# Kernel optimization log

Hardware: AMD Instinct MI355X
Metric: run time of the kernel (lower is better)

The kernel has to match this reference:

```python
import jax, jax.numpy as jnp
import numpy as np

IN_SLICE = (4, 4)   # input bit-plane widths, MSB first
W_SLICE = (4, 4)    # weight bit-plane widths, MSB first
KSIZE, STRIDE, PAD = 3, 1, 1
B, CIN, COUT, H, W = 16, 64, 128, 32, 32


def _slice_planes(x, bits):
    """Dynamic fixed-point quantization to sum(bits) signed bits, then split
    the magnitude into bit-planes (sign folded into each plane). Exact:
    sum_i 2**shift_i * plane_i == q, and scale * q ~= x."""
    n = int(sum(bits))
    qmax = float(2 ** (n - 1) - 1)
    scale = jnp.max(jnp.abs(x)) / qmax
    q = jnp.clip(jnp.round(x / scale), -qmax, qmax)
    sgn = jnp.sign(q)
    u = jnp.abs(q)
    planes, shifts = [], []
    s = n
    for b in bits:
        s -= b
        planes.append(sgn * (jnp.floor(u / (2.0 ** s)) % (2.0 ** b)))
        shifts.append(s)
    return planes, shifts, scale


def _unfold(x, k, stride, pad):
    """torch.nn.functional.unfold, (C, kh, kw) channel-major ordering.
    Returns [B, L, C*k*k], Ho, Wo."""
    b, c, h, w = x.shape
    xp = jnp.pad(x, ((0, 0), (0, 0), (pad, pad), (pad, pad)))
    ho = (h + 2 * pad - k) // stride + 1
    wo = (w + 2 * pad - k) // stride + 1
    cols = []
    for kh in range(k):
        for kw in range(k):
            cols.append(xp[:, :, kh:kh + (ho - 1) * stride + 1:stride,
                            kw:kw + (wo - 1) * stride + 1:stride])
    patches = jnp.stack(cols, axis=2)              # [B, C, k*k, Ho, Wo]
    patches = patches.reshape(b, c * k * k, ho * wo)
    return patches.transpose(0, 2, 1), ho, wo      # [B, L, K]


def _mem_conv(input, weight, bias):
    cout = weight.shape[0]
    wm = weight.reshape(cout, -1).T                # [K, Cout], matches weight.reshape(Cout,-1).t()
    xun, ho, wo = _unfold(input, KSIZE, STRIDE, PAD)
    xplanes, xshifts, xscale = _slice_planes(xun, IN_SLICE)
    wplanes, wshifts, wscale = _slice_planes(wm, W_SLICE)
    acc = jnp.zeros((input.shape[0], xun.shape[1], cout), dtype=input.dtype)
    for xp, sx in zip(xplanes, xshifts):
        for wp, sw in zip(wplanes, wshifts):
            # low-precision bit-plane GEMM with power-of-two shift recombination
            acc = acc + (2.0 ** (sx + sw)) * jnp.einsum('blk,ko->blo', xp, wp)
    out = (xscale * wscale) * acc                  # [B, L, Cout]
    out = out.transpose(0, 2, 1).reshape(input.shape[0], cout, ho, wo)
    return out + bias[None, :, None, None]


def setup_inputs() -> dict:
    key = jax.random.key(0)
    k1, k2, k3 = jax.random.split(key, 3)
    x = jax.random.normal(k1, (B, CIN, H, W), dtype=jnp.float32)
    fan_in = CIN * KSIZE * KSIZE
    bound = 1.0 / np.sqrt(fan_in)  # kaiming_uniform(a=sqrt(5)) -> U(-1/sqrt(fan_in), +)
    weight = jax.random.uniform(k2, (COUT, CIN, KSIZE, KSIZE), dtype=jnp.float32,
                                minval=-bound, maxval=bound)
    bias = jax.random.uniform(k3, (COUT,), dtype=jnp.float32, minval=-bound, maxval=bound)
    return {"input": x, "weight": weight, "bias": bias}


def reference(input, weight, bias):
    return _mem_conv(input, weight, bias)
```

## Files before the change

### kernel.cpp

```cpp
#include <hip/hip_runtime.h>

#define B_    16
#define CIN   64
#define COUT  128
#define H_    32
#define W_    32
#define HP    34
#define XCH   136
#define NPB   256

typedef __attribute__((ext_vector_type(4)))  int int4v;
typedef __attribute__((ext_vector_type(16))) int int16v;

__device__ __forceinline__ float wave_max256(const float* __restrict__ p) {
  const int lane = threadIdx.x & 63;
  float m = fmaxf(fmaxf(p[lane], p[lane + 64]),
                  fmaxf(p[lane + 128], p[lane + 192]));
#pragma unroll
  for (int off = 32; off > 0; off >>= 1)
    m = fmaxf(m, __shfl_down(m, off, 64));
  return __shfl(m, 0, 64);
}

__global__ __launch_bounds__(256) void maxabs_kernel(
    const float4* __restrict__ x4, const float4* __restrict__ w4,
    float* __restrict__ bmx, float* __restrict__ bmw) {
  const int nw4 = COUT * CIN * 9 / 4;
  const int tid = blockIdx.x * 256 + threadIdx.x;
  float mx = 0.0f, mw = 0.0f;
#pragma unroll
  for (int k = 0; k < 4; ++k) {
    float4 v = x4[tid + k * 65536];
    mx = fmaxf(mx, fmaxf(fmaxf(fabsf(v.x), fabsf(v.y)),
                         fmaxf(fabsf(v.z), fabsf(v.w))));
  }
  if (tid < nw4) {
    float4 v = w4[tid];
    mw = fmaxf(mw, fmaxf(fmaxf(fabsf(v.x), fabsf(v.y)),
                         fmaxf(fabsf(v.z), fabsf(v.w))));
  }
#pragma unroll
  for (int off = 32; off > 0; off >>= 1) {
    mx = fmaxf(mx, __shfl_down(mx, off, 64));
    mw = fmaxf(mw, __shfl_down(mw, off, 64));
  }
  __shared__ float smx[4], smw[4];
  const int wid = threadIdx.x >> 6;
  if ((threadIdx.x & 63) == 0) { smx[wid] = mx; smw[wid] = mw; }
  __syncthreads();
  if (threadIdx.x == 0) {
#pragma unroll
    for (int i = 1; i < 4; ++i) { mx = fmaxf(mx, smx[i]); mw = fmaxf(mw, smw[i]); }
    bmx[blockIdx.x] = mx;
    bmw[blockIdx.x] = mw;
  }
}

__global__ __launch_bounds__(256) void quant_pack_kernel(
    const float* __restrict__ x, const float* __restrict__ w,
    const float* __restrict__ bmx, const float* __restrict__ bmw,
    char* __restrict__ qx, char* __restrict__ qw) {
  __shared__ __align__(16) char lds[W_ * 80];
  const int t = threadIdx.x;
  const int bb = blockIdx.x;
  if (bb < 512) {
    const int b = bb >> 5, y = bb & 31;
    const float s = wave_max256(bmx) / 127.0f;
#pragma unroll
    for (int k = 0; k < 8; ++k) {
      const int u = t + k * 256;
      const int cin = u >> 5, xx = u & 31;
      float q = rintf(x[((b * CIN + cin) * H_ + y) * W_ + xx] / s);
      q = fminf(fmaxf(q, -127.0f), 127.0f);
      lds[xx * 80 + cin] = (char)(int)q;
    }
    __syncthreads();
    char* row = qx + (size_t)(b * HP + y + 1) * (XCH * 16);
    if (t < XCH) {
      const int c32 = t / 68;
      const int r   = t - c32 * 68;
      const int kb  = r / 34;
      const int xs  = r - kb * 34;
      uint4 v; v.x = v.y = v.z = v.w = 0;
      if (xs >= 1 && xs <= 32)
        v = *(const uint4*)(&lds[(xs - 1) * 80 + c32 * 32 + kb * 16]);
      *(uint4*)(row + t * 16) = v;
    }
  } else if (bb < 544) {
    const int idx = bb - 512;
    const int b = idx >> 1, yy = (idx & 1) ? 33 : 0;
    char* row = qx + (size_t)(b * HP + yy) * (XCH * 16);
    uint4 z; z.x = z.y = z.z = z.w = 0;
    if (t < XCH) *(uint4*)(row + t * 16) = z;
  } else {
    const int i = (bb - 544) * 256 + t;
    const float s = wave_max256(bmw) / 127.0f;
    float q = rintf(w[i] / s);
    q = fminf(fmaxf(q, -127.0f), 127.0f);
    const int kw = i % 3; int j = i / 3;
    const int kh = j % 3; j /= 3;
    const int c = j & 63; const int o = j >> 6;
    const int sidx = kh * 3 + kw;
    const int c32 = c >> 5, kb = (c >> 4) & 1, e = c & 15;
    qw[(size_t)(((sidx * 2 + c32) * 2 + kb) * 128 + o) * 16 + e] = (char)(int)q;
  }
}

__global__ __launch_bounds__(256, 2) void conv_mfma_kernel(
    const char* __restrict__ qx,
    const char* __restrict__ qw,
    const float* __restrict__ bmx, const float* __restrict__ bmw,
    const float* __restrict__ bias, float* __restrict__ out) {
  const int lane = threadIdx.x & 63;
  const int wv   = threadIdx.x >> 6;
  const int col  = lane & 31;
  const int kb   = lane >> 5;
  const int y    = blockIdx.x;
  const int b    = blockIdx.y;
  const int co0  = wv * 32;

  int16v acc0 = (int16v)0, acc1 = (int16v)0;

  const char* __restrict__ xp = qx + ((size_t)(b * HP + y) * 4 + kb) * 544 + col * 16;
  const char* __restrict__ wp = qw + (kb * 128 + co0 + col) * 16;

#pragma unroll
  for (int kh = 0; kh < 3; ++kh) {
    const char* __restrict__ xr = xp + (size_t)kh * (4 * 544);
#pragma unroll
    for (int kw = 0; kw < 3; ++kw) {
      const int s = kh * 3 + kw;
#pragma unroll
      for (int c32 = 0; c32 < 2; ++c32) {
        int4v a  = *(const int4v*)(wp + (s * 2 + c32) * 4096);
        int4v bf = *(const int4v*)(xr + c32 * 1088 + kw * 16);
        if (((s * 2 + c32) & 1) == 0)
          acc0 = __builtin_amdgcn_mfma_i32_32x32x32_i8(a, bf, acc0, 0, 0, 0);
        else
          acc1 = __builtin_amdgcn_mfma_i32_32x32x32_i8(a, bf, acc1, 0, 0, 0);
      }
    }
  }

  const float mx = wave_max256(bmx);
  const float mw = wave_max256(bmw);
  const float sc = (mx / 127.0f) * (mw / 127.0f);
#pragma unroll
  for (int r = 0; r < 16; ++r) {
    const int row  = (r & 3) + 8 * (r >> 2) + 4 * kb;
    const int cout = co0 + row;
    out[((b * COUT + cout) << 10) + y * W_ + col] =
        sc * (float)(acc0[r] + acc1[r]) + bias[cout];
  }
}

extern "C" void kernel_launch(void* const* d_in, const int* in_sizes, int n_in,
                              void* d_out, int out_size, void* d_ws, size_t ws_size,
                              hipStream_t stream) {
  const float* x    = (const float*)d_in[0];
  const float* w    = (const float*)d_in[1];
  const float* bias = (const float*)d_in[2];
  float* out = (float*)d_out;

  float* bmx = (float*)d_ws;
  float* bmw = bmx + 256;
  char* qx = (char*)d_ws + 2048;
  char* qw = qx + (size_t)B_ * HP * XCH * 16;

  maxabs_kernel<<<NPB, 256, 0, stream>>>((const float4*)x, (const float4*)w,
                                         bmx, bmw);
  quant_pack_kernel<<<832, 256, 0, stream>>>(x, w, bmx, bmw, qx, qw);
  conv_mfma_kernel<<<dim3(32, 16), 256, 0, stream>>>(qx, qw, bmx, bmw, bias, out);
}
```

Measured before the change: 68.66 us.

## Fuse max-abs, quantize/pack and MFMA conv into one cooperative kernel

Merges the three kernels (max-abs reduction, quantize/pack, int8 MFMA conv) into a single cooperative launch of 512 blocks, using grid-wide syncs between the phases. The aim is to remove two kernel launches and their inter-kernel gaps. Weight quantization and halo-row zeroing are spread across the same blocks. The cost is two grid.sync barriers, and the launch requires all 512 blocks to be co-resident.

```diff
diff --git a/kernel.cpp b/kernel.cpp
--- a/kernel.cpp
+++ b/kernel.cpp
@@ -1,4 +1,7 @@
 #include <hip/hip_runtime.h>
+#include <hip/hip_cooperative_groups.h>
+
+namespace cg = cooperative_groups;
 
 #define B_    16
 #define CIN   64
@@ -7,72 +10,97 @@
 #define W_    32
 #define HP    34
 #define XCH   136
-#define NPB   256
+#define NBLK  512
 
 typedef __attribute__((ext_vector_type(4)))  int int4v;
 typedef __attribute__((ext_vector_type(16))) int int16v;
 
-__device__ __forceinline__ float wave_max256(const float* __restrict__ p) {
-  const int lane = threadIdx.x & 63;
-  float m = fmaxf(fmaxf(p[lane], p[lane + 64]),
-                  fmaxf(p[lane + 128], p[lane + 192]));
+__global__ __launch_bounds__(256, 2) void fused_conv_kernel(
+    const float* __restrict__ x, const float* __restrict__ w,
+    const float* __restrict__ bias,
+    float* __restrict__ bmx, float* __restrict__ bmw,
+    char* __restrict__ qx,
+    char* __restrict__ qw,
+    float* __restrict__ out) {
+  cg::grid_group grid = cg::this_grid();
+
+  const int t    = threadIdx.x;
+  const int bb   = blockIdx.x;
+  const int lane = t & 63;
+  const int wid  = t >> 6;
+
+  __shared__ __align__(16) char lds[W_ * 80];
+  __shared__ float smx[4], smw[4];
+
+  {
+    const float4* __restrict__ x4 = (const float4*)x;
+    const float4* __restrict__ w4 = (const float4*)w;
+    const int g = bb * 256 + t;
+    float mx, mw = 0.0f;
+    float4 v0 = x4[g];
+    float4 v1 = x4[g + 131072];
+    mx = fmaxf(fmaxf(fmaxf(fabsf(v0.x), fabsf(v0.y)),
+                     fmaxf(fabsf(v0.z), fabsf(v0.w))),
+               fmaxf(fmaxf(fabsf(v1.x), fabsf(v1.y)),
+                     fmaxf(fabsf(v1.z), fabsf(v1.w))));
+    if (g < COUT * CIN * 9 / 4) {
+      float4 v = w4[g];
+      mw = fmaxf(fmaxf(fabsf(v.x), fabsf(v.y)),
+                 fmaxf(fabsf(v.z), fabsf(v.w)));
+    }
 #pragma unroll
-  for (int off = 32; off > 0; off >>= 1)
-    m = fmaxf(m, __shfl_down(m, off, 64));
-  return __shfl(m, 0, 64);
-}
+    for (int off = 32; off > 0; off >>= 1) {
+      mx = fmaxf(mx, __shfl_down(mx, off, 64));
+      mw = fmaxf(mw, __shfl_down(mw, off, 64));
+    }
+    if (lane == 0) { smx[wid] = mx; smw[wid] = mw; }
+    __syncthreads();
+    if (t == 0) {
+#pragma unroll
+      for (int i = 1; i < 4; ++i) { mx = fmaxf(mx, smx[i]); mw = fmaxf(mw, smw[i]); }
+      bmx[bb] = mx;
+      bmw[bb] = mw;
+    }
+  }
 
-__global__ __launch_bounds__(256) void maxabs_kernel(
-    const float4* __restrict__ x4, const float4* __restrict__ w4,
-    float* __restrict__ bmx, float* __restrict__ bmw) {
-  const int nw4 = COUT * CIN * 9 / 4;
-  const int tid = blockIdx.x * 256 + threadIdx.x;
-  float mx = 0.0f, mw = 0.0f;
+  grid.sync();
+
+  float gmx = 0.0f, gmw = 0.0f;
 #pragma unroll
-  for (int k = 0; k < 4; ++k) {
-    float4 v = x4[tid + k * 65536];
-    mx = fmaxf(mx, fmaxf(fmaxf(fabsf(v.x), fabsf(v.y)),
-                         fmaxf(fabsf(v.z), fabsf(v.w))));
-  }
-  if (tid < nw4) {
-    float4 v = w4[tid];
-    mw = fmaxf(mw, fmaxf(fmaxf(fabsf(v.x), fabsf(v.y)),
-                         fmaxf(fabsf(v.z), fabsf(v.w))));
+  for (int i = 0; i < 8; ++i) {
+    gmx = fmaxf(gmx, bmx[lane + 64 * i]);
+    gmw = fmaxf(gmw, bmw[lane + 64 * i]);
   }
 #pragma unroll
   for (int off = 32; off > 0; off >>= 1) {
-    mx = fmaxf(mx, __shfl_down(mx, off, 64));
-    mw = fmaxf(mw, __shfl_down(mw, off, 64));
+    gmx = fmaxf(gmx, __shfl_down(gmx, off, 64));
+    gmw = fmaxf(gmw, __shfl_down(gmw, off, 64));
   }
-  __shared__ float smx[4], smw[4];
-  const int wid = threadIdx.x >> 6;
-  if ((threadIdx.x & 63) == 0) { smx[wid] = mx; smw[wid] = mw; }
-  __syncthreads();
-  if (threadIdx.x == 0) {
-#pragma unroll
-    for (int i = 1; i < 4; ++i) { mx = fmaxf(mx, smx[i]); mw = fmaxf(mw, smw[i]); }
-    bmx[blockIdx.x] = mx;
-    bmw[blockIdx.x] = mw;
-  }
-}
+  gmx = __shfl(gmx, 0, 64);
+  gmw = __shfl(gmw, 0, 64);
+  const float sx = gmx / 127.0f;
+  const float sw = gmw / 127.0f;
 
-__global__ __launch_bounds__(256) void quant_pack_kernel(
-    const float* __restrict__ x, const float* __restrict__ w,
-    const float* __restrict__ bmx, const float* __restrict__ bmw,
-    char* __restrict__ qx, char* __restrict__ qw) {
-  __shared__ __align__(16) char lds[W_ * 80];
-  const int t = threadIdx.x;
-  const int bb = blockIdx.x;
-  if (bb < 512) {
-    const int b = bb >> 5, y = bb & 31;
-    const float s = wave_max256(bmx) / 127.0f;
+  const int b = bb >> 5, y = bb & 31;
+  {
 #pragma unroll
     for (int k = 0; k < 8; ++k) {
       const int u = t + k * 256;
       const int cin = u >> 5, xx = u & 31;
-      float q = rintf(x[((b * CIN + cin) * H_ + y) * W_ + xx] / s);
+      float q = rintf(x[((b * CIN + cin) * H_ + y) * W_ + xx] / sx);
       q = fminf(fmaxf(q, -127.0f), 127.0f);
       lds[xx * 80 + cin] = (char)(int)q;
+    }
+    if (t < 144) {
+      const int i = bb * 144 + t;
+      float q = rintf(w[i] / sw);
+      q = fminf(fmaxf(q, -127.0f), 127.0f);
+      const int kw = i % 3; int j = i / 3;
+      const int kh = j % 3; j /= 3;
+      const int c = j & 63; const int o = j >> 6;
+      const int sidx = kh * 3 + kw;
+      const int c32 = c >> 5, kb = (c >> 4) & 1, e = c & 15;
+      qw[(size_t)(((sidx * 2 + c32) * 2 + kb) * 128 + o) * 16 + e] = (char)(int)q;
     }
     __syncthreads();
     char* row = qx + (size_t)(b * HP + y + 1) * (XCH * 16);
@@ -86,71 +114,53 @@
         v = *(const uint4*)(&lds[(xs - 1) * 80 + c32 * 32 + kb * 16]);
       *(uint4*)(row + t * 16) = v;
     }
-  } else if (bb < 544) {
-    const int idx = bb - 512;
-    const int b = idx >> 1, yy = (idx & 1) ? 33 : 0;
-    char* row = qx + (size_t)(b * HP + yy) * (XCH * 16);
-    uint4 z; z.x = z.y = z.z = z.w = 0;
-    if (t < XCH) *(uint4*)(row + t * 16) = z;
-  } else {
-    const int i = (bb - 544) * 256 + t;
-    const float s = wave_max256(bmw) / 127.0f;
-    float q = rintf(w[i] / s);
-    q = fminf(fmaxf(q, -127.0f), 127.0f);
-    const int kw = i % 3; int j = i / 3;
-    const int kh = j % 3; j /= 3;
-    const int c = j & 63; const int o = j >> 6;
-    const int sidx = kh * 3 + kw;
-    const int c32 = c >> 5, kb = (c >> 4) & 1, e = c & 15;
-    qw[(size_t)(((sidx * 2 + c32) * 2 + kb) * 128 + o) * 16 + e] = (char)(int)q;
-  }
-}
-
-__global__ __launch_bounds__(256, 2) void conv_mfma_kernel(
-    const char* __restrict__ qx,
-    const char* __restrict__ qw,
-    const float* __restrict__ bmx, const float* __restrict__ bmw,
-    const float* __restrict__ bias, float* __restrict__ out) {
-  const int lane = threadIdx.x & 63;
-  const int wv   = threadIdx.x >> 6;
-  const int col  = lane & 31;
-  const int kb   = lane >> 5;
-  const int y    = blockIdx.x;
-  const int b    = blockIdx.y;
-  const int co0  = wv * 32;
-
-  int16v acc0 = (int16v)0, acc1 = (int16v)0;
-
-  const char* __restrict__ xp = qx + ((size_t)(b * HP + y) * 4 + kb) * 544 + col * 16;
-  const char* __restrict__ wp = qw + (kb * 128 + co0 + col) * 16;
-
-#pragma unroll
-  for (int kh = 0; kh < 3; ++kh) {
-    const char* __restrict__ xr = xp + (size_t)kh * (4 * 544);
-#pragma unroll
-    for (int kw = 0; kw < 3; ++kw) {
-      const int s = kh * 3 + kw;
-#pragma unroll
-      for (int c32 = 0; c32 < 2; ++c32) {
-        int4v a  = *(const int4v*)(wp + (s * 2 + c32) * 4096);
-        int4v bf = *(const int4v*)(xr + c32 * 1088 + kw * 16);
-        if (((s * 2 + c32) & 1) == 0)
-          acc0 = __builtin_amdgcn_mfma_i32_32x32x32_i8(a, bf, acc0, 0, 0, 0);
-        else
-          acc1 = __builtin_amdgcn_mfma_i32_32x32x32_i8(a, bf, acc1, 0, 0, 0);
-      }
+    if (bb < 32 && t < XCH) {
+      const int b2 = bb >> 1, yy = (bb & 1) ? 33 : 0;
+      char* hrow = qx + (size_t)(b2 * HP + yy) * (XCH * 16);
+      uint4 z; z.x = z.y = z.z = z.w = 0;
+      *(uint4*)(hrow + t * 16) = z;
     }
   }
 
-  const float mx = wave_max256(bmx);
-  const float mw = wave_max256(bmw);
-  const float sc = (mx / 127.0f) * (mw / 127.0f);
+  grid.sync();
+
+  {
+    const int col = lane & 31;
+    const int kb  = lane >> 5;
+    const int co0 = wid * 32;
+
+    int16v acc0 = (int16v)0, acc1 = (int16v)0;
+
+    const char* __restrict__ xp =
+        qx + ((size_t)(b * HP + y) * 4 + kb) * 544 + col * 16;
+    const char* __restrict__ wp = qw + (kb * 128 + co0 + col) * 16;
+
 #pragma unroll
-  for (int r = 0; r < 16; ++r) {
-    const int row  = (r & 3) + 8 * (r >> 2) + 4 * kb;
-    const int cout = co0 + row;
-    out[((b * COUT + cout) << 10) + y * W_ + col] =
-        sc * (float)(acc0[r] + acc1[r]) + bias[cout];
+    for (int kh = 0; kh < 3; ++kh) {
+      const char* __restrict__ xr = xp + (size_t)kh * (4 * 544);
+#pragma unroll
+      for (int kw = 0; kw < 3; ++kw) {
+        const int s = kh * 3 + kw;
+#pragma unroll
+        for (int c32 = 0; c32 < 2; ++c32) {
+          int4v a  = *(const int4v*)(wp + (s * 2 + c32) * 4096);
+          int4v bf = *(const int4v*)(xr + c32 * 1088 + kw * 16);
+          if (((s * 2 + c32) & 1) == 0)
+            acc0 = __builtin_amdgcn_mfma_i32_32x32x32_i8(a, bf, acc0, 0, 0, 0);
+          else
+            acc1 = __builtin_amdgcn_mfma_i32_32x32x32_i8(a, bf, acc1, 0, 0, 0);
+        }
+      }
+    }
+
+    const float sc = sx * sw;
+#pragma unroll
+    for (int r = 0; r < 16; ++r) {
+      const int row  = (r & 3) + 8 * (r >> 2) + 4 * kb;
+      const int cout = co0 + row;
+      out[((b * COUT + cout) << 10) + y * W_ + col] =
+          sc * (float)(acc0[r] + acc1[r]) + bias[cout];
+    }
   }
 }
 
@@ -163,12 +173,12 @@
   float* out = (float*)d_out;
 
   float* bmx = (float*)d_ws;
-  float* bmw = bmx + 256;
-  char* qx = (char*)d_ws + 2048;
+  float* bmw = bmx + 512;
+  char* qx = (char*)d_ws + 4096;
   char* qw = qx + (size_t)B_ * HP * XCH * 16;
 
-  maxabs_kernel<<<NPB, 256, 0, stream>>>((const float4*)x, (const float4*)w,
-                                         bmx, bmw);
-  quant_pack_kernel<<<832, 256, 0, stream>>>(x, w, bmx, bmw, qx, qw);
-  conv_mfma_kernel<<<dim3(32, 16), 256, 0, stream>>>(qx, qw, bmx, bmw, bias, out);
+  void* args[] = {(void*)&x, (void*)&w, (void*)&bias, (void*)&bmx,
+                  (void*)&bmw, (void*)&qx, (void*)&qw, (void*)&out};
+  hipLaunchCooperativeKernel((const void*)fused_conv_kernel,
+                             dim3(NBLK), dim3(256), args, 0, stream);
 }
```

Result: slower. 169.0 us (+146.1%).

## Fuse input quantization into conv kernel via LDS halo tiles

Applied to the files above, without the earlier changes.

Removes the separate input quantize/pack pass and its global int8 buffer. The conv kernel now reads fp32 input directly, quantizes a 6-row halo tile into shared memory, and runs MFMA from LDS. Blocks are retiled to 4 output rows by 32 output channels, one row per wave. This cuts a launch and a global round trip but re-reads and re-quantizes the input redundantly across cout quarters and halo rows.

```diff
diff --git a/kernel.cpp b/kernel.cpp
--- a/kernel.cpp
+++ b/kernel.cpp
@@ -5,8 +5,6 @@
 #define COUT  128
 #define H_    32
 #define W_    32
-#define HP    34
-#define XCH   136
 #define NPB   256
 
 typedef __attribute__((ext_vector_type(4)))  int int4v;
@@ -56,101 +54,102 @@
   }
 }
 
-__global__ __launch_bounds__(256) void quant_pack_kernel(
-    const float* __restrict__ x, const float* __restrict__ w,
-    const float* __restrict__ bmx, const float* __restrict__ bmw,
-    char* __restrict__ qx, char* __restrict__ qw) {
-  __shared__ __align__(16) char lds[W_ * 80];
-  const int t = threadIdx.x;
-  const int bb = blockIdx.x;
-  if (bb < 512) {
-    const int b = bb >> 5, y = bb & 31;
-    const float s = wave_max256(bmx) / 127.0f;
-#pragma unroll
-    for (int k = 0; k < 8; ++k) {
-      const int u = t + k * 256;
-      const int cin = u >> 5, xx = u & 31;
-      float q = rintf(x[((b * CIN + cin) * H_ + y) * W_ + xx] / s);
-      q = fminf(fmaxf(q, -127.0f), 127.0f);
-      lds[xx * 80 + cin] = (char)(int)q;
-    }
-    __syncthreads();
-    char* row = qx + (size_t)(b * HP + y + 1) * (XCH * 16);
-    if (t < XCH) {
-      const int c32 = t / 68;
-      const int r   = t - c32 * 68;
-      const int kb  = r / 34;
-      const int xs  = r - kb * 34;
-      uint4 v; v.x = v.y = v.z = v.w = 0;
-      if (xs >= 1 && xs <= 32)
-        v = *(const uint4*)(&lds[(xs - 1) * 80 + c32 * 32 + kb * 16]);
-      *(uint4*)(row + t * 16) = v;
-    }
-  } else if (bb < 544) {
-    const int idx = bb - 512;
-    const int b = idx >> 1, yy = (idx & 1) ? 33 : 0;
-    char* row = qx + (size_t)(b * HP + yy) * (XCH * 16);
-    uint4 z; z.x = z.y = z.z = z.w = 0;
-    if (t < XCH) *(uint4*)(row + t * 16) = z;
-  } else {
-    const int i = (bb - 544) * 256 + t;
-    const float s = wave_max256(bmw) / 127.0f;
-    float q = rintf(w[i] / s);
-    q = fminf(fmaxf(q, -127.0f), 127.0f);
-    const int kw = i % 3; int j = i / 3;
-    const int kh = j % 3; j /= 3;
-    const int c = j & 63; const int o = j >> 6;
-    const int sidx = kh * 3 + kw;
-    const int c32 = c >> 5, kb = (c >> 4) & 1, e = c & 15;
-    qw[(size_t)(((sidx * 2 + c32) * 2 + kb) * 128 + o) * 16 + e] = (char)(int)q;
-  }
+__global__ __launch_bounds__(256) void quantw_kernel(
+    const float* __restrict__ w, const float* __restrict__ bmw,
+    char* __restrict__ qw) {
+  const int i = blockIdx.x * 256 + threadIdx.x;
+  const float s = wave_max256(bmw) / 127.0f;
+  float q = rintf(w[i] / s);
+  q = fminf(fmaxf(q, -127.0f), 127.0f);
+  const int kw = i % 3; int j = i / 3;
+  const int kh = j % 3; j /= 3;
+  const int c = j & 63; const int o = j >> 6;
+  const int sidx = kh * 3 + kw;
+  const int c32 = c >> 5, kb = (c >> 4) & 1, e = c & 15;
+  qw[(size_t)(((sidx * 2 + c32) * 2 + kb) * 128 + o) * 16 + e] = (char)(int)q;
 }
 
-__global__ __launch_bounds__(256, 2) void conv_mfma_kernel(
-    const char* __restrict__ qx,
-    const char* __restrict__ qw,
+__global__ __launch_bounds__(256, 2) void conv_kernel(
+    const float* __restrict__ x, const char* __restrict__ qw,
     const float* __restrict__ bmx, const float* __restrict__ bmw,
     const float* __restrict__ bias, float* __restrict__ out) {
-  const int lane = threadIdx.x & 63;
-  const int wv   = threadIdx.x >> 6;
-  const int col  = lane & 31;
-  const int kb   = lane >> 5;
-  const int y    = blockIdx.x;
-  const int b    = blockIdx.y;
-  const int co0  = wv * 32;
+  const int t    = threadIdx.x;
+  const int bb   = blockIdx.x;
+  const int lane = t & 63;
+  const int wid  = t >> 6;
+  const int b  = bb >> 5;
+  const int yq = (bb >> 2) & 7;
+  const int cq = bb & 3;
 
-  int16v acc0 = (int16v)0, acc1 = (int16v)0;
-
-  const char* __restrict__ xp = qx + ((size_t)(b * HP + y) * 4 + kb) * 544 + col * 16;
-  const char* __restrict__ wp = qw + (kb * 128 + co0 + col) * 16;
-
-#pragma unroll
-  for (int kh = 0; kh < 3; ++kh) {
-    const char* __restrict__ xr = xp + (size_t)kh * (4 * 544);
-#pragma unroll
-    for (int kw = 0; kw < 3; ++kw) {
-      const int s = kh * 3 + kw;
-#pragma unroll
-      for (int c32 = 0; c32 < 2; ++c32) {
-        int4v a  = *(const int4v*)(wp + (s * 2 + c32) * 4096);
-        int4v bf = *(const int4v*)(xr + c32 * 1088 + kw * 16);
-        if (((s * 2 + c32) & 1) == 0)
-          acc0 = __builtin_amdgcn_mfma_i32_32x32x32_i8(a, bf, acc0, 0, 0, 0);
-        else
-          acc1 = __builtin_amdgcn_mfma_i32_32x32x32_i8(a, bf, acc1, 0, 0, 0);
-      }
-    }
-  }
+  __shared__ __align__(16) char qx_l[13056];
 
   const float mx = wave_max256(bmx);
   const float mw = wave_max256(bmw);
-  const float sc = (mx / 127.0f) * (mw / 127.0f);
+  const float sx = mx / 127.0f;
+
 #pragma unroll
-  for (int r = 0; r < 16; ++r) {
-    const int row  = (r & 3) + 8 * (r >> 2) + 4 * kb;
-    const int cout = co0 + row;
-    out[((b * COUT + cout) << 10) + y * W_ + col] =
-        sc * (float)(acc0[r] + acc1[r]) + bias[cout];
+  for (int k = 0; k < 4; ++k) {
+    const int ch = t + k * 256;
+    if (ch < 816) {
+      const int r = ch / 136, rem = ch - r * 136;
+      const int c32 = rem / 68, rem2 = rem - c32 * 68;
+      const int kb = rem2 / 34, xs = rem2 - kb * 34;
+      const int yy = yq * 4 - 1 + r;
+      const int xx = xs - 1;
+      unsigned d0 = 0, d1 = 0, d2 = 0, d3 = 0;
+      if (yy >= 0 && yy <= 31 && xx >= 0 && xx <= 31) {
+        const float* __restrict__ xp =
+            x + ((size_t)((b * CIN + c32 * 32 + kb * 16) * H_ + yy) * W_) + xx;
+#pragma unroll
+        for (int e = 0; e < 16; ++e) {
+          float q = rintf(xp[e * 1024] / sx);
+          q = fminf(fmaxf(q, -127.0f), 127.0f);
+          const unsigned byte = (unsigned)((int)q & 255) << ((e & 3) * 8);
+          if (e < 4) d0 |= byte; else if (e < 8) d1 |= byte;
+          else if (e < 12) d2 |= byte; else d3 |= byte;
+        }
+      }
+      int4v val = {(int)d0, (int)d1, (int)d2, (int)d3};
+      *(int4v*)(qx_l + (((r * 2 + c32) * 2 + kb) * 34 + xs) * 16) = val;
+    }
+  }
+  __syncthreads();
+
+  {
+    const int col = lane & 31;
+    const int kb  = lane >> 5;
+
+    int16v acc0 = (int16v)0, acc1 = (int16v)0;
+
+#pragma unroll
+    for (int kh = 0; kh < 3; ++kh) {
+      const int r = wid + kh;
+#pragma unroll
+      for (int kw = 0; kw < 3; ++kw) {
+        const int s = kh * 3 + kw;
+#pragma unroll
+        for (int c32 = 0; c32 < 2; ++c32) {
+          int4v a = *(const int4v*)(
+              qw + (size_t)(((s * 2 + c32) * 2 + kb) * 128 + cq * 32 + col) * 16);
+          int4v bf = *(const int4v*)(
+              qx_l + (((r * 2 + c32) * 2 + kb) * 34 + col + kw) * 16);
+          if (((s * 2 + c32) & 1) == 0)
+            acc0 = __builtin_amdgcn_mfma_i32_32x32x32_i8(a, bf, acc0, 0, 0, 0);
+          else
+            acc1 = __builtin_amdgcn_mfma_i32_32x32x32_i8(a, bf, acc1, 0, 0, 0);
+        }
+      }
+    }
+
+    const float sc = sx * (mw / 127.0f);
+    const int y = yq * 4 + wid;
+#pragma unroll
+    for (int rg = 0; rg < 16; ++rg) {
+      const int row  = (rg & 3) + 8 * (rg >> 2) + 4 * kb;
+      const int cout = cq * 32 + row;
+      out[((b * COUT + cout) << 10) + y * W_ + col] =
+          sc * (float)(acc0[rg] + acc1[rg]) + bias[cout];
+    }
   }
 }
 
@@ -164,11 +163,10 @@
 
   float* bmx = (float*)d_ws;
   float* bmw = bmx + 256;
-  char* qx = (char*)d_ws + 2048;
-  char* qw = qx + (size_t)B_ * HP * XCH * 16;
+  char* qw = (char*)d_ws + 2048;
 
   maxabs_kernel<<<NPB, 256, 0, stream>>>((const float4*)x, (const float4*)w,
                                          bmx, bmw);
-  quant_pack_kernel<<<832, 256, 0, stream>>>(x, w, bmx, bmw, qx, qw);
-  conv_mfma_kernel<<<dim3(32, 16), 256, 0, stream>>>(qx, qw, bmx, bmw, bias, out);
+  quantw_kernel<<<288, 256, 0, stream>>>(w, bmw, qw);
+  conv_kernel<<<512, 256, 0, stream>>>(x, qw, bmx, bmw, bias, out);
 }
```

After: 85.00 us. +23.8%, slower.
